# Performance work log

Hardware: AMD Instinct MI355X
Metric: run time of the kernel (lower is better)

The kernel has to match this reference:

```python
import jax, jax.numpy as jnp
import numpy as np

B, T, D = 2, 4096, 1024
H, HD = 16, 64
KV = H * HD  # 1024


def setup_inputs() -> dict:
    key = jax.random.key(0)
    ks = jax.random.split(key, 6)
    sc = lambda k, shape, s: jax.random.normal(k, shape, jnp.float32) * s
    return {
        "x": sc(ks[0], (B, T, D), 1.0),
        "W_in": sc(ks[1], (D, 4 * KV), D ** -0.5),      # in_proj (in, out) layout
        "W_ba": sc(ks[2], (D, 2 * H), D ** -0.5),       # ba_proj
        "conv_w": sc(ks[3], (3 * KV, 1, 4), 0.5),       # depthwise conv, (O, I/groups=1, K)
        "dt_bias": jnp.ones((H,), jnp.float32),
        "A_log": jnp.log(jax.random.uniform(ks[4], (H,), jnp.float32, 1e-3, 16.0)),
        "norm_w": jnp.ones((HD,), jnp.float32),
        "W_o": sc(ks[5], (KV, D), KV ** -0.5),
    }


def _l2norm(t, eps=1e-6):
    return t * jax.lax.rsqrt(jnp.sum(t * t, axis=-1, keepdims=True) + eps)


def reference(x, W_in, W_ba, conv_w, dt_bias, A_log, norm_w, W_o):
    Bb, Tt, _ = x.shape
    qkvz = x @ W_in                                  # [B,T,4*KV]
    q, k, v, z = jnp.split(qkvz, 4, axis=-1)
    b, a = jnp.split(x @ W_ba, 2, axis=-1)           # [B,T,H] each

    # causal depthwise conv (kernel 4, left pad 3) + SiLU on concat(q,k,v)
    qkv = jnp.concatenate([q, k, v], axis=-1).transpose(0, 2, 1)  # [B,3KV,T]
    qkv = jax.lax.conv_general_dilated(
        qkv, conv_w, window_strides=(1,), padding=[(3, 0)],
        feature_group_count=3 * KV, dimension_numbers=("NCH", "OIH", "NCH"))
    qkv = jax.nn.silu(qkv).transpose(0, 2, 1)        # [B,T,3KV]
    q, k, v = jnp.split(qkv, 3, axis=-1)

    rs = lambda t: t.reshape(Bb, Tt, H, HD)
    q, k, v, z = rs(q), rs(k), rs(v), rs(z)

    beta = jax.nn.sigmoid(b)                         # [B,T,H]
    A = jnp.exp(jnp.maximum(A_log, -2.3))            # [H]
    g = -A * jax.nn.softplus(a + dt_bias)            # [B,T,H], log decay <= 0

    # fla use_qk_l2norm_in_kernel=True: l2-normalize q,k; q scaled by d^-0.5
    q = _l2norm(q) * (HD ** -0.5)
    k = _l2norm(k)

    # gated delta rule recurrence over time (state S: [B,H,dk,dv])
    tm = lambda t: jnp.swapaxes(t, 0, 1)             # time-major

    def step(S, inp):
        qt, kt, vt, gt, bt = inp
        S = S * jnp.exp(gt)[..., None, None]
        pred = jnp.einsum("bhk,bhkv->bhv", kt, S)
        S = S + jnp.einsum("bhk,bhv->bhkv", kt, (vt - pred) * bt[..., None])
        o = jnp.einsum("bhk,bhkv->bhv", qt, S)
        return S, o

    S0 = jnp.zeros((Bb, H, HD, HD), jnp.float32)
    _, y = jax.lax.scan(step, S0, (tm(q), tm(k), tm(v), tm(g), tm(beta)))
    y = jnp.swapaxes(y, 0, 1)                        # [B,T,H,HD]

    # RMSNormGated over head_dim, gated by silu(z)
    y = y * jax.lax.rsqrt(jnp.mean(y * y, axis=-1, keepdims=True) + 1e-6)
    y = (norm_w * y) * jax.nn.silu(z)

    return y.reshape(Bb, Tt, KV) @ W_o
```

## Files before the change

kernel.cpp:

```cpp
#include <hip/hip_runtime.h>

typedef unsigned short u16;
typedef unsigned int u32;
typedef __attribute__((ext_vector_type(8))) __bf16 bf16x8;
typedef __attribute__((ext_vector_type(8))) _Float16 f16x8;
typedef __attribute__((ext_vector_type(4))) _Float16 f16x4;
typedef __attribute__((ext_vector_type(4))) float f32x4;

#define DEV __device__ __forceinline__

DEV u16 f2bf(float f) {
  u32 u = __float_as_uint(f);
  u += 0x7FFFu + ((u >> 16) & 1u);
  return (u16)(u >> 16);
}
DEV float bf2f(u16 h) { return __uint_as_float(((u32)h) << 16); }
DEV void splitbf(float f, u16& hi, u16& lo) {
  u16 h = f2bf(f);
  hi = h;
  lo = f2bf(f - bf2f(h));
}
DEV void split4(float4 v, ushort4& hh, ushort4& ll) {
  splitbf(v.x, hh.x, ll.x);
  splitbf(v.y, hh.y, ll.y);
  splitbf(v.z, hh.z, ll.z);
  splitbf(v.w, hh.w, ll.w);
}
DEV int SW(int r, int c) { return r * 64 + ((c) ^ ((r & 7) << 3)); }

DEV int SWG(int r, int c) {
  int db = ((r & 1) << 2) | ((c >> 3) & 3);
  int dbp = db ^ ((r >> 1) & 7);
  return ((r >> 1) << 6) | (dbp << 3) | (c & 7);
}
DEV size_t gidx_swz(size_t row, int col, int rowlen) {
  int rr7 = (int)((row >> 1) & 7);
  int db = (int)(((row & 1) << 2) | ((col >> 3) & 3));
  int dbp = db ^ rr7;
  size_t rowp = (row & ~(size_t)1) | (size_t)(dbp >> 2);
  int colp = (col & ~31) | ((dbp & 3) << 3) | (col & 7);
  return rowp * (size_t)rowlen + colp;
}

#define MFMA16(a,b,c) __builtin_amdgcn_mfma_f32_16x16x32_bf16((a),(b),(c),0,0,0)
#define MFMAH(a,b,c)  __builtin_amdgcn_mfma_f32_16x16x32_f16((a),(b),(c),0,0,0)
#define GLDS16(g,l) __builtin_amdgcn_global_load_lds((__attribute__((address_space(1))) void*)(g), (__attribute__((address_space(3))) void*)(l), 16, 0, 0)

DEV f32x4 mm3(bf16x8 ah, bf16x8 al, bf16x8 bh, bf16x8 bl, f32x4 acc) {
  acc = MFMA16(ah, bl, acc);
  acc = MFMA16(al, bh, acc);
  acc = MFMA16(ah, bh, acc);
  return acc;
}

__global__ __launch_bounds__(256) void k_cast_h(const float* __restrict__ in, _Float16* __restrict__ out, int n) {
  int idx = (blockIdx.x * 256 + threadIdx.x) * 4;
  if (idx + 3 < n) {
    float4 v = *(const float4*)(in + idx);
    f16x4 o = {(_Float16)v.x, (_Float16)v.y, (_Float16)v.z, (_Float16)v.w};
    const size_t row = (size_t)(idx >> 10);
    const int col = idx & 1023;
    *(f16x4*)(out + gidx_swz(row, col, 1024)) = o;
  }
}

__global__ __launch_bounds__(256) void k_transpose_h(const float* __restrict__ in, _Float16* __restrict__ out, int R, int Cc) {
  __shared__ float tile[64][65];
  int c0 = blockIdx.x * 64, r0 = blockIdx.y * 64;
  int lr = threadIdx.x >> 6, lc = threadIdx.x & 63;
#pragma unroll
  for (int i = 0; i < 16; ++i) {
    int r = lr + i * 4;
    tile[r][lc] = in[(size_t)(r0 + r) * Cc + c0 + lc];
  }
  __syncthreads();
#pragma unroll
  for (int i = 0; i < 16; ++i) {
    int oc = lr + i * 4;
    out[gidx_swz((size_t)(c0 + oc), r0 + lc, R)] = (_Float16)tile[lc][oc];
  }
}

__global__ __launch_bounds__(256) void k_transpose(const float* __restrict__ in, u16* __restrict__ out, int R, int Cc) {
  __shared__ float tile[64][65];
  int c0 = blockIdx.x * 64, r0 = blockIdx.y * 64;
  int lr = threadIdx.x >> 6, lc = threadIdx.x & 63;
#pragma unroll
  for (int i = 0; i < 16; ++i) {
    int r = lr + i * 4;
    tile[r][lc] = in[(size_t)(r0 + r) * Cc + c0 + lc];
  }
  __syncthreads();
#pragma unroll
  for (int i = 0; i < 16; ++i) {
    int oc = lr + i * 4;
    out[gidx_swz((size_t)(c0 + oc), r0 + lc, R)] = f2bf(tile[lc][oc]);
  }
}

__global__ __launch_bounds__(512, 2) void k_gemm_h(const _Float16* __restrict__ A, const _Float16* __restrict__ Bt,
                                                   u16* __restrict__ Cq, u16* __restrict__ Cz, int M, int N, int K) {
  __shared__ __align__(16) u16 As[256 * 32];
  __shared__ __align__(16) u16 Bs[256 * 32];
  const int tid = threadIdx.x;
  const int nwg = gridDim.x * gridDim.y;
  int bid = blockIdx.y * gridDim.x + blockIdx.x;
  bid = (bid & 7) * (nwg >> 3) + (bid >> 3);
  const int m0 = (bid / gridDim.x) * 256, n0 = (bid % gridDim.x) * 256;
  const int w = tid >> 6, l = tid & 63;
  const int wr = (w >> 1) * 64, wc = (w & 1) * 128;
  const int lrow = l & 15, lk = (l >> 4) * 8, rbase = (l >> 4) * 4;

  f32x4 acc[4][8];
#pragma unroll
  for (int i = 0; i < 4; ++i)
#pragma unroll
    for (int j = 0; j < 8; ++j) acc[i][j] = {0.f, 0.f, 0.f, 0.f};

  const _Float16* aBase = A + (size_t)m0 * K;
  const _Float16* bBase = Bt + (size_t)n0 * K;
  const int srow0 = tid >> 2, scol0 = (tid & 3) * 8;
  const int srow1 = (tid + 512) >> 2;

  for (int k0 = 0; k0 < K; k0 += 32) {
    __syncthreads();
    GLDS16(aBase + (size_t)srow0 * K + k0 + scol0, &As[tid * 8]);
    GLDS16(aBase + (size_t)srow1 * K + k0 + scol0, &As[4096 + tid * 8]);
    GLDS16(bBase + (size_t)srow0 * K + k0 + scol0, &Bs[tid * 8]);
    GLDS16(bBase + (size_t)srow1 * K + k0 + scol0, &Bs[4096 + tid * 8]);
    __syncthreads();
    f16x8 af[4], bfr[8];
#pragma unroll
    for (int i = 0; i < 4; ++i) af[i] = *(const f16x8*)&As[SWG(wr + i * 16 + lrow, lk)];
#pragma unroll
    for (int j = 0; j < 8; ++j) bfr[j] = *(const f16x8*)&Bs[SWG(wc + j * 16 + lrow, lk)];
#pragma unroll
    for (int i = 0; i < 4; ++i)
#pragma unroll
      for (int j = 0; j < 8; ++j) acc[i][j] = MFMAH(af[i], bfr[j], acc[i][j]);
  }
#pragma unroll
  for (int i = 0; i < 4; ++i)
#pragma unroll
    for (int j = 0; j < 8; ++j)
#pragma unroll
      for (int r = 0; r < 4; ++r) {
        int row = m0 + wr + i * 16 + rbase + r;
        int col = n0 + wc + j * 16 + lrow;
        if (col < 3072) Cq[(size_t)row * 3072 + col] = f2bf(acc[i][j][r]);
        else            Cz[(size_t)row * 1024 + col - 3072] = f2bf(acc[i][j][r]);
      }
}

__global__ __launch_bounds__(256) void k_gemm2(const u16* __restrict__ Ah, const u16* __restrict__ Al,
                                               const u16* __restrict__ Bt, float* __restrict__ Cf,
                                               int M, int N, int K) {
  __shared__ __align__(16) u16 Ash[128 * 32];
  __shared__ __align__(16) u16 Asl[128 * 32];
  __shared__ __align__(16) u16 Bs[128 * 32];
  const int tid = threadIdx.x;
  const int nwg = gridDim.x * gridDim.y;
  int bid = blockIdx.y * gridDim.x + blockIdx.x;
  bid = (bid & 7) * (nwg >> 3) + (bid >> 3);
  const int m0 = (bid / gridDim.x) * 128, n0 = (bid % gridDim.x) * 128;
  const int w = tid >> 6, l = tid & 63;
  const int wr = (w >> 1) * 64, wc = (w & 1) * 64;
  const int lrow = l & 15, lk = (l >> 4) * 8, rbase = (l >> 4) * 4;
  const int srow = tid >> 2, scol = (tid & 3) * 8;

  f32x4 acc[4][4];
#pragma unroll
  for (int i = 0; i < 4; ++i)
#pragma unroll
    for (int j = 0; j < 4; ++j) acc[i][j] = {0.f, 0.f, 0.f, 0.f};

  const u16* ahBase = Ah + (size_t)m0 * K;
  const u16* alBase = Al + (size_t)m0 * K;
  const u16* bBase  = Bt + (size_t)n0 * K;

  for (int k0 = 0; k0 < K; k0 += 32) {
    __syncthreads();
    GLDS16(ahBase + (size_t)srow * K + k0 + scol,        &Ash[tid * 8]);
    GLDS16(ahBase + (size_t)(srow + 64) * K + k0 + scol, &Ash[2048 + tid * 8]);
    GLDS16(alBase + (size_t)srow * K + k0 + scol,        &Asl[tid * 8]);
    GLDS16(alBase + (size_t)(srow + 64) * K + k0 + scol, &Asl[2048 + tid * 8]);
    GLDS16(bBase + (size_t)srow * K + k0 + scol,         &Bs[tid * 8]);
    GLDS16(bBase + (size_t)(srow + 64) * K + k0 + scol,  &Bs[2048 + tid * 8]);
    __syncthreads();
    bf16x8 afh[4], afl[4], bfr[4];
#pragma unroll
    for (int i = 0; i < 4; ++i) afh[i] = *(const bf16x8*)&Ash[SWG(wr + i * 16 + lrow, lk)];
#pragma unroll
    for (int i = 0; i < 4; ++i) afl[i] = *(const bf16x8*)&Asl[SWG(wr + i * 16 + lrow, lk)];
#pragma unroll
    for (int j = 0; j < 4; ++j) bfr[j] = *(const bf16x8*)&Bs[SWG(wc + j * 16 + lrow, lk)];
#pragma unroll
    for (int i = 0; i < 4; ++i)
#pragma unroll
      for (int j = 0; j < 4; ++j) {
        acc[i][j] = MFMA16(afl[i], bfr[j], acc[i][j]);
        acc[i][j] = MFMA16(afh[i], bfr[j], acc[i][j]);
      }
  }
#pragma unroll
  for (int i = 0; i < 4; ++i)
#pragma unroll
    for (int j = 0; j < 4; ++j)
#pragma unroll
      for (int r = 0; r < 4; ++r) {
        int row = m0 + wr + i * 16 + rbase + r;
        int col = n0 + wc + j * 16 + lrow;
        Cf[(size_t)row * N + col] = acc[i][j][r];
      }
}

__global__ __launch_bounds__(256) void k_ba(const float* __restrict__ x, const float* __restrict__ Wba,
                                            const float* __restrict__ dt_bias, const float* __restrict__ A_log,
                                            float* __restrict__ betaO, float* __restrict__ gO) {
  __shared__ float xs[4][1024];
  const int wid = threadIdx.x >> 6, lane = threadIdx.x & 63;
  const int m = blockIdx.x * 4 + wid;
#pragma unroll
  for (int i = 0; i < 16; ++i) xs[wid][lane + 64 * i] = x[(size_t)m * 1024 + lane + 64 * i];
  __syncthreads();
  const int n = lane & 31, half = lane >> 5;
  float acc = 0.f;
  const float* wp = Wba + n;
  const int kk0 = half * 512;
#pragma unroll 8
  for (int kk = kk0; kk < kk0 + 512; ++kk) acc += xs[wid][kk] * wp[kk * 32];
  acc += __shfl_xor(acc, 32);
  if (lane < 32) {
    if (n < 16) {
      betaO[(size_t)m * 16 + n] = 1.f / (1.f + expf(-acc));
    } else {
      int h = n - 16;
      float xx = acc + dt_bias[h];
      float sp = (xx > 20.f) ? xx : log1pf(expf(xx));
      gO[(size_t)m * 16 + h] = -expf(fmaxf(A_log[h], -2.3f)) * sp;
    }
  }
}

__global__ __launch_bounds__(256) void k_conv(const u16* __restrict__ qkv3, const float* __restrict__ convw,
                                              u16* __restrict__ qhG, u16* __restrict__ qlG,
                                              u16* __restrict__ khG, u16* __restrict__ klG,
                                              u16* __restrict__ vhG, u16* __restrict__ vlG) {
  __shared__ float cs[3072];
  __shared__ float innorm[32];
  const int bt = blockIdx.x;
  const int bb = bt >> 12, tt = bt & 4095;
  const int tid = threadIdx.x;
  const size_t rb = (size_t)bb * 4096;
#pragma unroll
  for (int s = 0; s < 3; ++s) {
    const int c4 = tid * 4 + s * 1024;
    float cwa[4][4];
#pragma unroll
    for (int e = 0; e < 4; ++e) {
      float4 t = *(const float4*)&convw[(c4 + e) * 4];
      cwa[e][0] = t.x; cwa[e][1] = t.y; cwa[e][2] = t.z; cwa[e][3] = t.w;
    }
    float acc[4] = {0.f, 0.f, 0.f, 0.f};
#pragma unroll
    for (int j = 0; j < 4; ++j) {
      const int tau = tt - 3 + j;
      if (tau >= 0) {
        ushort4 kv = *(const ushort4*)&qkv3[(rb + tau) * 3072 + c4];
        acc[0] += bf2f(kv.x) * cwa[0][j];
        acc[1] += bf2f(kv.y) * cwa[1][j];
        acc[2] += bf2f(kv.z) * cwa[2][j];
        acc[3] += bf2f(kv.w) * cwa[3][j];
      }
    }
#pragma unroll
    for (int e = 0; e < 4; ++e) cs[c4 + e] = acc[e] / (1.f + expf(-acc[e]));
  }
  __syncthreads();
  {
    const int grp = tid >> 3, off = (tid & 7) * 8;
    const float* p = cs + grp * 64 + off;
    float s = 0.f;
#pragma unroll
    for (int i = 0; i < 8; ++i) s += p[i] * p[i];
    s += __shfl_xor(s, 1); s += __shfl_xor(s, 2); s += __shfl_xor(s, 4);
    if ((tid & 7) == 0) innorm[grp] = rsqrtf(s + 1e-6f);
  }
  __syncthreads();
  const int h = tid >> 4, d4 = (tid & 15) * 4;
  const size_t ob = ((size_t)(bb * 16 + h) * 64 + (tt >> 6)) * 4096 + SW(tt & 63, d4);
  {
    const int ci = h * 64 + d4;
    const float sc = innorm[h] * 0.125f;
    float4 o = {cs[ci] * sc, cs[ci + 1] * sc, cs[ci + 2] * sc, cs[ci + 3] * sc};
    ushort4 hh, ll;
    split4(o, hh, ll);
    *(ushort4*)&qhG[ob] = hh;
    *(ushort4*)&qlG[ob] = ll;
  }
  {
    const int ci = 1024 + h * 64 + d4;
    const float sc = innorm[16 + h];
    float4 o = {cs[ci] * sc, cs[ci + 1] * sc, cs[ci + 2] * sc, cs[ci + 3] * sc};
    ushort4 hh, ll;
    split4(o, hh, ll);
    *(ushort4*)&khG[ob] = hh;
    *(ushort4*)&klG[ob] = ll;
  }
  {
    const int ci = 2048 + h * 64 + d4;
    float4 o = {cs[ci], cs[ci + 1], cs[ci + 2], cs[ci + 3]};
    ushort4 hh, ll;
    split4(o, hh, ll);
    *(ushort4*)&vhG[ob] = hh;
    *(ushort4*)&vlG[ob] = ll;
  }
}

__global__ __launch_bounds__(64) void k_prep(const u16* __restrict__ khG, const u16* __restrict__ klG,
                                             const float* __restrict__ gG, const float* __restrict__ betaG,
                                             float* __restrict__ gcG, u16* __restrict__ Tgh, u16* __restrict__ Tgl) {
  __shared__ __align__(16) char pmem[16384];
  u16* Kbh = (u16*)pmem;
  u16* Kbl = (u16*)(pmem + 8192);
  float* Af = (float*)pmem;
  __shared__ float gcs[64], bs[64];
  const int bhc = blockIdx.x;
  const int c = bhc & 63, h = (bhc >> 6) & 15, bb = bhc >> 10;
  const int lane = threadIdx.x;
  const int t0 = c * 64;
  const size_t rowbase = (size_t)bb * 4096;
  const size_t ktile = (size_t)bhc * 4096;
#pragma unroll
  for (int i = 0; i < 8; ++i) {
    const int idx = lane + 64 * i;
    GLDS16(khG + ktile + idx * 8, &Kbh[idx * 8]);
    GLDS16(klG + ktile + idx * 8, &Kbl[idx * 8]);
  }
  {
    float gv = gG[(rowbase + t0 + lane) * 16 + h];
    float sc = gv;
#pragma unroll
    for (int off = 1; off < 64; off <<= 1) {
      float o = __shfl_up(sc, off);
      if (lane >= off) sc += o;
    }
    gcs[lane] = sc;
    bs[lane] = betaG[(rowbase + t0 + lane) * 16 + h];
    gcG[(size_t)bhc * 64 + lane] = sc;
  }
  __syncthreads();
  const int lrow = lane & 15, lk8 = (lane >> 4) * 8, rbase = (lane >> 4) * 4;
  f32x4 acc[4][4];
#pragma unroll
  for (int i = 0; i < 4; ++i)
#pragma unroll
    for (int j = 0; j < 4; ++j) acc[i][j] = {0.f, 0.f, 0.f, 0.f};
#pragma unroll
  for (int ks = 0; ks < 2; ++ks) {
    bf16x8 afh[4], afl[4], bfh[4], bfl[4];
#pragma unroll
    for (int i = 0; i < 4; ++i) {
      afh[i] = *(const bf16x8*)&Kbh[SW(i * 16 + lrow, ks * 32 + lk8)];
      afl[i] = *(const bf16x8*)&Kbl[SW(i * 16 + lrow, ks * 32 + lk8)];
    }
#pragma unroll
    for (int j = 0; j < 4; ++j) {
      bfh[j] = *(const bf16x8*)&Kbh[SW(j * 16 + lrow, ks * 32 + lk8)];
      bfl[j] = *(const bf16x8*)&Kbl[SW(j * 16 + lrow, ks * 32 + lk8)];
    }
#pragma unroll
    for (int i = 0; i < 4; ++i)
#pragma unroll
      for (int j = 0; j < 4; ++j) acc[i][j] = mm3(afh[i], afl[i], bfh[j], bfl[j], acc[i][j]);
  }
  __syncthreads();
#pragma unroll
  for (int i = 0; i < 4; ++i)
#pragma unroll
    for (int j = 0; j < 4; ++j)
#pragma unroll
      for (int r = 0; r < 4; ++r) {
        int t = i * 16 + rbase + r, s = j * 16 + lrow;
        Af[t * 64 + s] = (s < t) ? bs[t] * expf(gcs[t] - gcs[s]) * acc[i][j][r] : 0.f;
      }
  __syncthreads();
  float x[64];
#pragma unroll
  for (int t = 0; t < 64; ++t) {
    float sum = 0.f;
#pragma unroll
    for (int s4 = 0; s4 + 4 <= t; s4 += 4) {
      float4 a4 = *(const float4*)&Af[t * 64 + s4];
      sum += a4.x * x[s4] + a4.y * x[s4 + 1] + a4.z * x[s4 + 2] + a4.w * x[s4 + 3];
    }
#pragma unroll
    for (int s = (t & ~3); s < t; ++s) sum += Af[t * 64 + s] * x[s];
    x[t] = ((t == lane) ? 1.f : 0.f) - sum;
  }
#pragma unroll
  for (int t = 0; t < 64; ++t) {
    u16 hi, lo;
    splitbf(x[t], hi, lo);
    Tgh[(size_t)bhc * 4096 + SW(t, lane)] = hi;
    Tgl[(size_t)bhc * 4096 + SW(t, lane)] = lo;
  }
}

__global__ __launch_bounds__(256) void k_mn(const u16* __restrict__ khG, const u16* __restrict__ klG,
                                            const u16* __restrict__ vhG, const u16* __restrict__ vlG,
                                            const u16* __restrict__ Tgh, const u16* __restrict__ Tgl,
                                            const float* __restrict__ gcG, const float* __restrict__ betaG,
                                            u16* __restrict__ Mh, u16* __restrict__ Ml,
                                            u16* __restrict__ Nh, u16* __restrict__ Nl) {
  extern __shared__ __align__(16) char smem[];
  u16* base = (u16*)smem;
  u16* Tbh  = base + 0 * 4096;
  u16* Tbl  = base + 1 * 4096;
  u16* X1h  = base + 2 * 4096;
  u16* X1l  = base + 3 * 4096;
  u16* KdTh = base + 4 * 4096;
  u16* KdTl = base + 5 * 4096;
  u16* X2h  = base + 6 * 4096;
  u16* X2l  = base + 7 * 4096;
  float* gcs = (float*)(base + 8 * 4096);
  float* bs  = gcs + 64;

  const int bhc = blockIdx.x;
  const int c = bhc & 63, h = (bhc >> 6) & 15, bb = bhc >> 10;
  const int tid = threadIdx.x, w = tid >> 6, l = tid & 63;
  const int lrow = l & 15, lk8 = (l >> 4) * 8, rbase = (l >> 4) * 4;
  const int t0 = c * 64;
  const size_t rowbase = (size_t)bb * 4096;
  const size_t ktile = (size_t)bhc * 4096;

  if (tid < 64) {
    gcs[tid] = gcG[(size_t)bhc * 64 + tid];
    bs[tid] = betaG[(rowbase + t0 + tid) * 16 + h];
  }
#pragma unroll
  for (int i = 0; i < 2; ++i) {
    const int idx = tid + 256 * i;
    const int off = idx * 8;
    *(float4*)&Tbh[off] = *(const float4*)&Tgh[(size_t)bhc * 4096 + off];
    *(float4*)&Tbl[off] = *(const float4*)&Tgl[(size_t)bhc * 4096 + off];
  }
  __syncthreads();
  const float gc63 = gcs[63];
#pragma unroll
  for (int i = 0; i < 16; ++i) {
    const int flat = tid + 256 * i;
    const int s = flat >> 6, d = flat & 63;
    const int sws = SW(s, d);
    const float kf = bf2f(khG[ktile + sws]) + bf2f(klG[ktile + sws]);
    const float gv = gcs[s], bv = bs[s];
    u16 hh, ll;
    splitbf(bv * expf(gv) * kf, hh, ll);
    X1h[SW(d, s)] = hh; X1l[SW(d, s)] = ll;
    splitbf(expf(gc63 - gv) * kf, hh, ll);
    KdTh[SW(d, s)] = hh; KdTl[SW(d, s)] = ll;
    const float vv = bf2f(vhG[ktile + sws]) + bf2f(vlG[ktile + sws]);
    splitbf(bv * vv, hh, ll);
    X2h[SW(d, s)] = hh; X2l[SW(d, s)] = ll;
  }
  __syncthreads();

  f32x4 aW[4], aU[4];
#pragma unroll
  for (int j = 0; j < 4; ++j) { aW[j] = {0.f,0.f,0.f,0.f}; aU[j] = {0.f,0.f,0.f,0.f}; }
#pragma unroll
  for (int ks = 0; ks < 2; ++ks) {
    const int ao = SW(w * 16 + lrow, ks * 32 + lk8);
    bf16x8 aTh = *(const bf16x8*)&Tbh[ao];
    bf16x8 aTl = *(const bf16x8*)&Tbl[ao];
#pragma unroll
    for (int j = 0; j < 4; ++j) {
      const int bo = SW(j * 16 + lrow, ks * 32 + lk8);
      aW[j] = mm3(aTh, aTl, *(const bf16x8*)&X1h[bo], *(const bf16x8*)&X1l[bo], aW[j]);
      aU[j] = mm3(aTh, aTl, *(const bf16x8*)&X2h[bo], *(const bf16x8*)&X2l[bo], aU[j]);
    }
  }
  __syncthreads();
#pragma unroll
  for (int j = 0; j < 4; ++j)
#pragma unroll
    for (int r = 0; r < 4; ++r) {
      const int t = w * 16 + rbase + r, dcol = j * 16 + lrow;
      u16 hh, ll;
      splitbf(aW[j][r], hh, ll);
      X1h[SW(dcol, t)] = hh; X1l[SW(dcol, t)] = ll;
      splitbf(aU[j][r], hh, ll);
      X2h[SW(dcol, t)] = hh; X2l[SW(dcol, t)] = ll;
    }
  __syncthreads();

  f32x4 aM[4], aN[4];
#pragma unroll
  for (int j = 0; j < 4; ++j) { aM[j] = {0.f,0.f,0.f,0.f}; aN[j] = {0.f,0.f,0.f,0.f}; }
#pragma unroll
  for (int ks = 0; ks < 2; ++ks) {
    const int ao = SW(w * 16 + lrow, ks * 32 + lk8);
    bf16x8 aKh = *(const bf16x8*)&KdTh[ao];
    bf16x8 aKl = *(const bf16x8*)&KdTl[ao];
#pragma unroll
    for (int j = 0; j < 4; ++j) {
      const int bo = SW(j * 16 + lrow, ks * 32 + lk8);
      aM[j] = mm3(aKh, aKl, *(const bf16x8*)&X1h[bo], *(const bf16x8*)&X1l[bo], aM[j]);
      aN[j] = mm3(aKh, aKl, *(const bf16x8*)&X2h[bo], *(const bf16x8*)&X2l[bo], aN[j]);
    }
  }
  __syncthreads();
  const float decC = expf(gc63);
#pragma unroll
  for (int j = 0; j < 4; ++j)
#pragma unroll
    for (int r = 0; r < 4; ++r) {
      const int d = w * 16 + rbase + r, d2 = j * 16 + lrow;
      u16 hh, ll;
      splitbf(((d == d2) ? decC : 0.f) - aM[j][r], hh, ll);
      X1h[SW(d, d2)] = hh; X1l[SW(d, d2)] = ll;
      splitbf(aN[j][r], hh, ll);
      X2h[SW(d, d2)] = hh; X2l[SW(d, d2)] = ll;
    }
  __syncthreads();
#pragma unroll
  for (int i = 0; i < 2; ++i) {
    const int idx = tid + 256 * i;
    const int off = idx * 8;
    *(float4*)&Mh[(size_t)bhc * 4096 + off] = *(const float4*)&X1h[off];
    *(float4*)&Ml[(size_t)bhc * 4096 + off] = *(const float4*)&X1l[off];
    *(float4*)&Nh[(size_t)bhc * 4096 + off] = *(const float4*)&X2h[off];
    *(float4*)&Nl[(size_t)bhc * 4096 + off] = *(const float4*)&X2l[off];
  }
}

__global__ __launch_bounds__(256) void k_seg(const u16* __restrict__ Mh, const u16* __restrict__ Ml,
                                             const u16* __restrict__ Nh, const u16* __restrict__ Nl,
                                             u16* __restrict__ Msegh, u16* __restrict__ Msegl,
                                             u16* __restrict__ Nsegh, u16* __restrict__ Nsegl) {
  extern __shared__ __align__(16) char smem[];
  u16* base = (u16*)smem;
  u16* MaTh = base + 0 * 4096;
  u16* MaTl = base + 1 * 4096;
  u16* NaTh = base + 2 * 4096;
  u16* NaTl = base + 3 * 4096;
  u16* sMh  = base + 4 * 4096;
  u16* sMl  = base + 5 * 4096;
  u16* sNh  = base + 6 * 4096;
  u16* sNl  = base + 7 * 4096;

  const int blk = blockIdx.x;
  const size_t cbase = (size_t)(blk >> 3) * 64 + (blk & 7) * 8;
  const int tid = threadIdx.x, w = tid >> 6, l = tid & 63;
  const int lrow = l & 15, lk8 = (l >> 4) * 8, rbase = (l >> 4) * 4;

#pragma unroll
  for (int i = 0; i < 2; ++i) {
    const int off = (tid + 256 * i) * 8;
    *(float4*)&sMh[off] = *(const float4*)&Mh[cbase * 4096 + off];
    *(float4*)&sMl[off] = *(const float4*)&Ml[cbase * 4096 + off];
    *(float4*)&sNh[off] = *(const float4*)&Nh[cbase * 4096 + off];
    *(float4*)&sNl[off] = *(const float4*)&Nl[cbase * 4096 + off];
  }
  __syncthreads();
#pragma unroll
  for (int i = 0; i < 16; ++i) {
    const int flat = tid + 256 * i;
    const int a = flat >> 6, b = flat & 63;
    MaTh[SW(a, b)] = sMh[SW(b, a)];
    MaTl[SW(a, b)] = sMl[SW(b, a)];
    NaTh[SW(a, b)] = sNh[SW(b, a)];
    NaTl[SW(a, b)] = sNl[SW(b, a)];
  }
  __syncthreads();

  for (int j = 1; j < 8; ++j) {
#pragma unroll
    for (int i = 0; i < 2; ++i) {
      const int off = (tid + 256 * i) * 8;
      *(float4*)&sMh[off] = *(const float4*)&Mh[(cbase + j) * 4096 + off];
      *(float4*)&sMl[off] = *(const float4*)&Ml[(cbase + j) * 4096 + off];
      *(float4*)&sNh[off] = *(const float4*)&Nh[(cbase + j) * 4096 + off];
      *(float4*)&sNl[off] = *(const float4*)&Nl[(cbase + j) * 4096 + off];
    }
    __syncthreads();
    f32x4 aM2[4], aN2[4];
#pragma unroll
    for (int jj = 0; jj < 4; ++jj) { aM2[jj] = {0.f,0.f,0.f,0.f}; aN2[jj] = {0.f,0.f,0.f,0.f}; }
#pragma unroll
    for (int ks = 0; ks < 2; ++ks) {
      const int ao = SW(w * 16 + lrow, ks * 32 + lk8);
      bf16x8 aCh = *(const bf16x8*)&sMh[ao];
      bf16x8 aCl = *(const bf16x8*)&sMl[ao];
#pragma unroll
      for (int jj = 0; jj < 4; ++jj) {
        const int bo = SW(jj * 16 + lrow, ks * 32 + lk8);
        aM2[jj] = mm3(aCh, aCl, *(const bf16x8*)&MaTh[bo], *(const bf16x8*)&MaTl[bo], aM2[jj]);
        aN2[jj] = mm3(aCh, aCl, *(const bf16x8*)&NaTh[bo], *(const bf16x8*)&NaTl[bo], aN2[jj]);
      }
    }
    __syncthreads();
#pragma unroll
    for (int jj = 0; jj < 4; ++jj)
#pragma unroll
      for (int r = 0; r < 4; ++r) {
        const int t = w * 16 + rbase + r, col = jj * 16 + lrow;
        u16 hh, ll;
        splitbf(aM2[jj][r], hh, ll);
        MaTh[SW(col, t)] = hh; MaTl[SW(col, t)] = ll;
        const float nv = aN2[jj][r] + bf2f(sNh[SW(t, col)]) + bf2f(sNl[SW(t, col)]);
        splitbf(nv, hh, ll);
        NaTh[SW(col, t)] = hh; NaTl[SW(col, t)] = ll;
      }
    __syncthreads();
  }
#pragma unroll
  for (int i = 0; i < 16; ++i) {
    const int flat = tid + 256 * i;
    const int t = flat >> 6, s = flat & 63;
    Msegh[(size_t)blk * 4096 + SW(t, s)] = MaTh[SW(s, t)];
    Msegl[(size_t)blk * 4096 + SW(t, s)] = MaTl[SW(s, t)];
    Nsegh[(size_t)blk * 4096 + SW(t, s)] = NaTh[SW(s, t)];
    Nsegl[(size_t)blk * 4096 + SW(t, s)] = NaTl[SW(s, t)];
  }
}

__global__ __launch_bounds__(256) void k_bound(const u16* __restrict__ Msegh, const u16* __restrict__ Msegl,
                                               const u16* __restrict__ Nsegh, const u16* __restrict__ Nsegl,
                                               u16* __restrict__ Ssegh, u16* __restrict__ Ssegl) {
  __shared__ __align__(16) u16 STh[4096], STl[4096];
  __shared__ __align__(16) u16 sMh[4096], sMl[4096], sNh[4096], sNl[4096];
  const int bh = blockIdx.x;
  const int tid = threadIdx.x, w = tid >> 6, l = tid & 63;
  const int lrow = l & 15, lk8 = (l >> 4) * 8, rbase = (l >> 4) * 4;
  for (int i = tid; i < 4096; i += 256) { STh[i] = (u16)0; STl[i] = (u16)0; }
  __syncthreads();
  for (int j = 0; j < 8; ++j) {
    const size_t sb = (size_t)(bh * 8 + j) * 4096;
#pragma unroll
    for (int i = 0; i < 2; ++i) {
      const int off = (tid + 256 * i) * 8;
      *(float4*)&Ssegh[sb + off] = *(const float4*)&STh[off];
      *(float4*)&Ssegl[sb + off] = *(const float4*)&STl[off];
      *(float4*)&sMh[off] = *(const float4*)&Msegh[sb + off];
      *(float4*)&sMl[off] = *(const float4*)&Msegl[sb + off];
      *(float4*)&sNh[off] = *(const float4*)&Nsegh[sb + off];
      *(float4*)&sNl[off] = *(const float4*)&Nsegl[sb + off];
    }
    __syncthreads();
    f32x4 acc[4];
#pragma unroll
    for (int jj = 0; jj < 4; ++jj) acc[jj] = {0.f, 0.f, 0.f, 0.f};
#pragma unroll
    for (int ks = 0; ks < 2; ++ks) {
      const int ao = SW(w * 16 + lrow, ks * 32 + lk8);
      bf16x8 aSh = *(const bf16x8*)&STh[ao];
      bf16x8 aSl = *(const bf16x8*)&STl[ao];
#pragma unroll
      for (int jj = 0; jj < 4; ++jj) {
        const int bo = SW(jj * 16 + lrow, ks * 32 + lk8);
        acc[jj] = mm3(aSh, aSl, *(const bf16x8*)&sMh[bo], *(const bf16x8*)&sMl[bo], acc[jj]);
      }
    }
    __syncthreads();
#pragma unroll
    for (int jj = 0; jj < 4; ++jj)
#pragma unroll
      for (int r = 0; r < 4; ++r) {
        const int v = w * 16 + rbase + r, t = jj * 16 + lrow;
        const float sv = acc[jj][r] + bf2f(sNh[SW(t, v)]) + bf2f(sNl[SW(t, v)]);
        u16 hh, ll;
        splitbf(sv, hh, ll);
        STh[SW(v, t)] = hh; STl[SW(v, t)] = ll;
      }
    __syncthreads();
  }
}

__global__ __launch_bounds__(512, 2) void k_scan2(const u16* __restrict__ qhG, const u16* __restrict__ qlG,
                                               const u16* __restrict__ khG, const u16* __restrict__ klG,
                                               const u16* __restrict__ vhG, const u16* __restrict__ vlG,
                                               const u16* __restrict__ zb,
                                               const u16* __restrict__ Tgh, const u16* __restrict__ Tgl,
                                               const float* __restrict__ gcG,
                                               const float* __restrict__ betaG, const float* __restrict__ norm_w,
                                               const u16* __restrict__ Ssegh, const u16* __restrict__ Ssegl,
                                               u16* __restrict__ Yhi, u16* __restrict__ Ylo) {
  extern __shared__ __align__(16) char smem[];
  u16* base = (u16*)smem;
  u16* Kbh  = base + 0 * 4096;
  u16* Kbl  = base + 1 * 4096;
  u16* Qbh  = base + 2 * 4096;
  u16* Qbl  = base + 3 * 4096;
  u16* Vbh  = base + 4 * 4096;
  u16* Vbl  = base + 5 * 4096;
  u16* Zb   = base + 6 * 4096;
  u16* Tbh  = base + 7 * 4096;
  u16* Tbl  = base + 8 * 4096;
  u16* SbTh = base + 9 * 4096;
  u16* SbTl = base + 10 * 4096;
  u16* Mqh  = base + 11 * 4096;
  u16* Mql  = base + 12 * 4096;
  u16* KdTh = base + 13 * 4096;
  u16* KdTl = base + 14 * 4096;
  u16* RTh  = base + 15 * 4096;
  u16* RTl  = base + 16 * 4096;
  u16* UTh  = base + 17 * 4096;
  u16* UTl  = base + 18 * 4096;
  u16* Ybh  = RTh;
  u16* Ybl  = RTl;
  float* gcs = (float*)(base + 19 * 4096);
  float* bs  = gcs + 64;
  float* nws = gcs + 128;
  float* esF = gcs + 192;
  float* etF = gcs + 256;
  float* ssP = gcs + 320;

  const int blk = blockIdx.x;
  const int bh = blk >> 3, seg = blk & 7;
  const int bb = bh >> 4, h = bh & 15;
  const int tid = threadIdx.x, w = tid >> 6, l = tid & 63;
  const int wrow = w >> 1, jh = w & 1;
  const int lrow = l & 15, lk8 = (l >> 4) * 8, rbase = (l >> 4) * 4;
  const size_t rowbase = (size_t)bb * 4096;
  const size_t bhTile = (size_t)bh * 64;
  const int o8 = tid * 8;
  const int zr = tid >> 3, zc8 = (tid & 7) << 3;

  {
    const int c = seg * 8, t0 = c * 64;
    const size_t gt = (bhTile + c) * 4096;
    GLDS16(qhG + gt + o8, &Qbh[o8]);
    GLDS16(qlG + gt + o8, &Qbl[o8]);
    GLDS16(khG + gt + o8, &Kbh[o8]);
    GLDS16(klG + gt + o8, &Kbl[o8]);
    GLDS16(vhG + gt + o8, &Vbh[o8]);
    GLDS16(vlG + gt + o8, &Vbl[o8]);
    GLDS16(Tgh + (size_t)(bh * 64 + c) * 4096 + o8, &Tbh[o8]);
    GLDS16(Tgl + (size_t)(bh * 64 + c) * 4096 + o8, &Tbl[o8]);
    GLDS16(Ssegh + (size_t)blk * 4096 + o8, &SbTh[o8]);
    GLDS16(Ssegl + (size_t)blk * 4096 + o8, &SbTl[o8]);
    *(float4*)&Zb[SW(zr, zc8)] = *(const float4*)&zb[(rowbase + t0 + zr) * 1024 + h * 64 + zc8];
    if (tid < 64) {
      nws[tid] = norm_w[tid];
      float g0 = gcG[((size_t)bh * 64 + c) * 64 + tid];
      float b0 = betaG[(rowbase + t0 + tid) * 16 + h];
      float g63 = __shfl(g0, 63);
      gcs[tid] = g0; bs[tid] = b0;
      esF[tid] = expf(g63 - g0);
      etF[tid] = expf(g0);
    }
  }
  __syncthreads();

  for (int cc = 0; cc < 8; ++cc) {
    const int c = seg * 8 + cc;
    const int t0 = c * 64;
    const bool pf = (cc < 7);
    const size_t gt1 = (bhTile + c + 1) * 4096;

    float4 pz;
    float pgc = 0.f, pbs = 0.f;
    if (pf) {
      const int t1 = t0 + 64;
      pz = *(const float4*)&zb[(rowbase + t1 + zr) * 1024 + h * 64 + zc8];
      if (tid < 64) {
        pgc = gcG[((size_t)bh * 64 + (c + 1)) * 64 + tid];
        pbs = betaG[(rowbase + t1 + tid) * 16 + h];
      }
    }

#pragma unroll
    for (int i = 0; i < 8; ++i) {
      const int flat = tid * 8 + i;
      const int d = flat >> 6, s = flat & 63;
      const float kv = bf2f(Kbh[SW(s, d)]) + bf2f(Kbl[SW(s, d)]);
      u16 hh, ll;
      splitbf(esF[s] * kv, hh, ll);
      KdTh[SW(d, s)] = hh;
      KdTl[SW(d, s)] = ll;
    }
    f32x4 aqk[2], ap[2], aqs[2];
#pragma unroll
    for (int j = 0; j < 2; ++j) { aqk[j] = {0.f,0.f,0.f,0.f}; ap[j] = {0.f,0.f,0.f,0.f}; aqs[j] = {0.f,0.f,0.f,0.f}; }
#pragma unroll
    for (int ks = 0; ks < 2; ++ks) {
      const int ao = SW(wrow * 16 + lrow, ks * 32 + lk8);
      bf16x8 aKh = *(const bf16x8*)&Kbh[ao];
      bf16x8 aKl = *(const bf16x8*)&Kbl[ao];
      bf16x8 aQh = *(const bf16x8*)&Qbh[ao];
      bf16x8 aQl = *(const bf16x8*)&Qbl[ao];
#pragma unroll
      for (int j = 0; j < 2; ++j) {
        const int jj = jh * 2 + j;
        const int bo = SW(jj * 16 + lrow, ks * 32 + lk8);
        bf16x8 bKh = *(const bf16x8*)&Kbh[bo];
        bf16x8 bKl = *(const bf16x8*)&Kbl[bo];
        bf16x8 bSh = *(const bf16x8*)&SbTh[bo];
        bf16x8 bSl = *(const bf16x8*)&SbTl[bo];
        aqk[j] = mm3(aQh, aQl, bKh, bKl, aqk[j]);
        ap[j]  = mm3(aKh, aKl, bSh, bSl, ap[j]);
        aqs[j] = mm3(aQh, aQl, bSh, bSl, aqs[j]);
      }
    }
#pragma unroll
    for (int j = 0; j < 2; ++j)
#pragma unroll
      for (int r = 0; r < 4; ++r) {
        const int t = wrow * 16 + rbase + r;
        const int s = (jh * 2 + j) * 16 + lrow;
        u16 mh, ml;
        splitbf((s <= t) ? expf(gcs[t] - gcs[s]) * aqk[j][r] : 0.f, mh, ml);
        Mqh[SW(t, s)] = mh;
        Mql[SW(t, s)] = ml;
        const float vv = bf2f(Vbh[SW(t, s)]) + bf2f(Vbl[SW(t, s)]);
        const float rhs = bs[t] * (vv - etF[t] * ap[j][r]);
        u16 rh, rl;
        splitbf(rhs, rh, rl);
        RTh[SW(s, t)] = rh;
        RTl[SW(s, t)] = rl;
      }
    __syncthreads();

    if (pf) {
      GLDS16(qhG + gt1 + o8, &Qbh[o8]);
      GLDS16(qlG + gt1 + o8, &Qbl[o8]);
      GLDS16(khG + gt1 + o8, &Kbh[o8]);
      GLDS16(klG + gt1 + o8, &Kbl[o8]);
      GLDS16(vhG + gt1 + o8, &Vbh[o8]);
      GLDS16(vlG + gt1 + o8, &Vbl[o8]);
    }

    f32x4 au[2];
#pragma unroll
    for (int j = 0; j < 2; ++j) au[j] = {0.f, 0.f, 0.f, 0.f};
#pragma unroll
    for (int ks = 0; ks < 2; ++ks) {
      const int ao = SW(wrow * 16 + lrow, ks * 32 + lk8);
      bf16x8 aTh = *(const bf16x8*)&Tbh[ao];
      bf16x8 aTl = *(const bf16x8*)&Tbl[ao];
#pragma unroll
      for (int j = 0; j < 2; ++j) {
        const int bo = SW((jh * 2 + j) * 16 + lrow, ks * 32 + lk8);
        au[j] = mm3(aTh, aTl, *(const bf16x8*)&RTh[bo], *(const bf16x8*)&RTl[bo], au[j]);
      }
    }
#pragma unroll
    for (int j = 0; j < 2; ++j)
#pragma unroll
      for (int r = 0; r < 4; ++r) {
        u16 uh, ul;
        splitbf(au[j][r], uh, ul);
        const int o = SW((jh * 2 + j) * 16 + lrow, wrow * 16 + rbase + r);
        UTh[o] = uh;
        UTl[o] = ul;
      }
    __syncthreads();

    if (pf) {
      GLDS16(Tgh + (size_t)(bh * 64 + (c + 1)) * 4096 + o8, &Tbh[o8]);
      GLDS16(Tgl + (size_t)(bh * 64 + (c + 1)) * 4096 + o8, &Tbl[o8]);
    }

    f32x4 amu[2], as_[2];
#pragma unroll
    for (int j = 0; j < 2; ++j) { amu[j] = {0.f,0.f,0.f,0.f}; as_[j] = {0.f,0.f,0.f,0.f}; }
#pragma unroll
    for (int ks = 0; ks < 2; ++ks) {
      const int ao = SW(wrow * 16 + lrow, ks * 32 + lk8);
      bf16x8 aMh = *(const bf16x8*)&Mqh[ao];
      bf16x8 aMl = *(const bf16x8*)&Mql[ao];
      bf16x8 aKdh = *(const bf16x8*)&KdTh[ao];
      bf16x8 aKdl = *(const bf16x8*)&KdTl[ao];
#pragma unroll
      for (int j = 0; j < 2; ++j) {
        const int bo = SW((jh * 2 + j) * 16 + lrow, ks * 32 + lk8);
        bf16x8 bUh = *(const bf16x8*)&UTh[bo];
        bf16x8 bUl = *(const bf16x8*)&UTl[bo];
        amu[j] = mm3(aMh, aMl, bUh, bUl, amu[j]);
        as_[j] = mm3(aKdh, aKdl, bUh, bUl, as_[j]);
      }
    }
    float yv_[4][2];
#pragma unroll
    for (int r = 0; r < 4; ++r) {
      const int t = wrow * 16 + rbase + r;
      const float gt = etF[t];
      float ss = 0.f;
#pragma unroll
      for (int j = 0; j < 2; ++j) {
        yv_[r][j] = gt * aqs[j][r] + amu[j][r];
        ss += yv_[r][j] * yv_[r][j];
      }
      ss += __shfl_xor(ss, 1); ss += __shfl_xor(ss, 2); ss += __shfl_xor(ss, 4); ss += __shfl_xor(ss, 8);
      if (lrow == 0) ssP[jh * 64 + t] = ss;
    }
    __syncthreads();
#pragma unroll
    for (int r = 0; r < 4; ++r) {
      const int t = wrow * 16 + rbase + r;
      const float rstd = rsqrtf((ssP[t] + ssP[64 + t]) * (1.f / 64.f) + 1e-6f);
#pragma unroll
      for (int j = 0; j < 2; ++j) {
        const int col = (jh * 2 + j) * 16 + lrow;
        const float zz = bf2f(Zb[SW(t, col)]);
        const float yv = yv_[r][j] * rstd * nws[col] * (zz / (1.f + expf(-zz)));
        u16 yh, yl;
        splitbf(yv, yh, yl);
        Ybh[SW(t, col)] = yh;
        Ybl[SW(t, col)] = yl;
      }
    }
    {
      const float decC = etF[63];
#pragma unroll
      for (int j = 0; j < 2; ++j)
#pragma unroll
        for (int r = 0; r < 4; ++r) {
          const int d = wrow * 16 + rbase + r, col = (jh * 2 + j) * 16 + lrow;
          const int o = SW(col, d);
          const float s0 = bf2f(SbTh[o]) + bf2f(SbTl[o]);
          const float sv = decC * s0 + as_[j][r];
          u16 sh, sl;
          splitbf(sv, sh, sl);
          SbTh[o] = sh;
          SbTl[o] = sl;
        }
    }
    __syncthreads();

    {
      const size_t gsw = gidx_swz(rowbase + t0 + zr, h * 64 + zc8, 1024);
      *(float4*)&Yhi[gsw] = *(const float4*)&Ybh[SW(zr, zc8)];
      *(float4*)&Ylo[gsw] = *(const float4*)&Ybl[SW(zr, zc8)];
    }
    if (pf) {
      *(float4*)&Zb[SW(zr, zc8)] = pz;
      if (tid < 64) {
        float g63 = __shfl(pgc, 63);
        gcs[tid] = pgc; bs[tid] = pbs;
        esF[tid] = expf(g63 - pgc);
        etF[tid] = expf(pgc);
      }
    }
    __syncthreads();
  }
}

extern "C" void kernel_launch(void* const* d_in, const int* in_sizes, int n_in,
                              void* d_out, int out_size, void* d_ws, size_t ws_size,
                              hipStream_t stream) {
  (void)in_sizes; (void)n_in; (void)out_size; (void)ws_size;
  const float* x       = (const float*)d_in[0];
  const float* W_in    = (const float*)d_in[1];
  const float* W_ba    = (const float*)d_in[2];
  const float* conv_w  = (const float*)d_in[3];
  const float* dt_bias = (const float*)d_in[4];
  const float* A_log   = (const float*)d_in[5];
  const float* norm_w  = (const float*)d_in[6];
  const float* W_o     = (const float*)d_in[7];
  float* out = (float*)d_out;
  char* ws = (char*)d_ws;
  const size_t MB = 1048576;

  _Float16* xh = (_Float16*)(ws + 0);
  u16* MhB   = (u16*)(ws + 0);
  u16* YhiB  = (u16*)(ws + 0);
  u16* MlB   = (u16*)(ws + 16 * MB);
  u16* YloB  = (u16*)(ws + 16 * MB);
  _Float16* WinT = (_Float16*)(ws + 32 * MB);
  float* gB  = (float*)(ws + 32 * MB);
  float* bB  = (float*)(ws + 32 * MB + 524288);
  float* gcB = (float*)(ws + 33 * MB);
  u16* Ssegh = (u16*)(ws + 34 * MB);
  u16* Ssegl = (u16*)(ws + 36 * MB);
  u16* Msegh = (u16*)(ws + 38 * MB);
  u16* Msegl = (u16*)(ws + 40 * MB);
  u16* Nsegh = (u16*)(ws + 42 * MB);
  u16* Nsegl = (u16*)(ws + 44 * MB);
  u16* WoT   = (u16*)(ws + 48 * MB);
  u16* qkv3  = (u16*)(ws + 50 * MB);
  u16* NhB   = (u16*)(ws + 50 * MB);
  u16* NlB   = (u16*)(ws + 66 * MB);
  u16* zbB   = (u16*)(ws + 98 * MB);
  u16* qhG   = (u16*)(ws + 114 * MB);
  u16* qlG   = (u16*)(ws + 130 * MB);
  u16* khG   = (u16*)(ws + 146 * MB);
  u16* klG   = (u16*)(ws + 162 * MB);
  u16* vhG   = (u16*)(ws + 178 * MB);
  u16* vlG   = (u16*)(ws + 194 * MB);
  u16* TghB  = (u16*)(ws + 210 * MB);
  u16* TglB  = (u16*)(ws + 226 * MB);

  const int SCAN_LDS = 19 * 8192 + 448 * 4;
  const int MN_LDS   = 8 * 8192 + 512;
  const int SEG_LDS  = 8 * 8192;

  k_cast_h<<<8192, 256, 0, stream>>>(x, xh, 8388608);
  k_transpose_h<<<dim3(64, 16), 256, 0, stream>>>(W_in, WinT, 1024, 4096);
  k_transpose<<<dim3(16, 16), 256, 0, stream>>>(W_o, WoT, 1024, 1024);
  k_gemm_h<<<dim3(16, 32), 512, 0, stream>>>(xh, WinT, qkv3, zbB, 8192, 4096, 1024);
  k_ba<<<2048, 256, 0, stream>>>(x, W_ba, dt_bias, A_log, bB, gB);
  k_conv<<<8192, 256, 0, stream>>>(qkv3, conv_w, qhG, qlG, khG, klG, vhG, vlG);
  k_prep<<<2048, 64, 0, stream>>>(khG, klG, gB, bB, gcB, TghB, TglB);
  hipFuncSetAttribute((const void*)k_mn, hipFuncAttributeMaxDynamicSharedMemorySize, MN_LDS);
  k_mn<<<2048, 256, MN_LDS, stream>>>(khG, klG, vhG, vlG, TghB, TglB, gcB, bB, MhB, MlB, NhB, NlB);
  hipFuncSetAttribute((const void*)k_seg, hipFuncAttributeMaxDynamicSharedMemorySize, SEG_LDS);
  k_seg<<<256, 256, SEG_LDS, stream>>>(MhB, MlB, NhB, NlB, Msegh, Msegl, Nsegh, Nsegl);
  k_bound<<<32, 256, 0, stream>>>(Msegh, Msegl, Nsegh, Nsegl, Ssegh, Ssegl);
  hipFuncSetAttribute((const void*)k_scan2, hipFuncAttributeMaxDynamicSharedMemorySize, SCAN_LDS);
  k_scan2<<<256, 512, SCAN_LDS, stream>>>(qhG, qlG, khG, klG, vhG, vlG, zbB, TghB, TglB, gcB, bB, norm_w,
                                          Ssegh, Ssegl, YhiB, YloB);
  k_gemm2<<<dim3(8, 64), 256, 0, stream>>>(YhiB, YloB, WoT, out, 8192, 1024, 1024);
}
```

Measured before the change: 530.9 us.

## Double-buffer LDS tiles in both GEMM kernels to overlap loads with MFMA

```diff
diff --git a/kernel.cpp b/kernel.cpp
--- a/kernel.cpp
+++ b/kernel.cpp
@@ -100,8 +100,8 @@
 
 __global__ __launch_bounds__(512, 2) void k_gemm_h(const _Float16* __restrict__ A, const _Float16* __restrict__ Bt,
                                                    u16* __restrict__ Cq, u16* __restrict__ Cz, int M, int N, int K) {
-  __shared__ __align__(16) u16 As[256 * 32];
-  __shared__ __align__(16) u16 Bs[256 * 32];
+  __shared__ __align__(16) u16 As[2][256 * 32];
+  __shared__ __align__(16) u16 Bs[2][256 * 32];
   const int tid = threadIdx.x;
   const int nwg = gridDim.x * gridDim.y;
   int bid = blockIdx.y * gridDim.x + blockIdx.x;
@@ -122,22 +122,29 @@
   const int srow0 = tid >> 2, scol0 = (tid & 3) * 8;
   const int srow1 = (tid + 512) >> 2;
 
+  auto STAGE = [&](int buf, int k0) {
+    GLDS16(aBase + (size_t)srow0 * K + k0 + scol0, &As[buf][tid * 8]);
+    GLDS16(aBase + (size_t)srow1 * K + k0 + scol0, &As[buf][4096 + tid * 8]);
+    GLDS16(bBase + (size_t)srow0 * K + k0 + scol0, &Bs[buf][tid * 8]);
+    GLDS16(bBase + (size_t)srow1 * K + k0 + scol0, &Bs[buf][4096 + tid * 8]);
+  };
+
+  STAGE(0, 0);
+  __syncthreads();
+  int cur = 0;
   for (int k0 = 0; k0 < K; k0 += 32) {
-    __syncthreads();
-    GLDS16(aBase + (size_t)srow0 * K + k0 + scol0, &As[tid * 8]);
-    GLDS16(aBase + (size_t)srow1 * K + k0 + scol0, &As[4096 + tid * 8]);
-    GLDS16(bBase + (size_t)srow0 * K + k0 + scol0, &Bs[tid * 8]);
-    GLDS16(bBase + (size_t)srow1 * K + k0 + scol0, &Bs[4096 + tid * 8]);
-    __syncthreads();
+    if (k0 + 32 < K) STAGE(cur ^ 1, k0 + 32);
     f16x8 af[4], bfr[8];
 #pragma unroll
-    for (int i = 0; i < 4; ++i) af[i] = *(const f16x8*)&As[SWG(wr + i * 16 + lrow, lk)];
-#pragma unroll
-    for (int j = 0; j < 8; ++j) bfr[j] = *(const f16x8*)&Bs[SWG(wc + j * 16 + lrow, lk)];
+    for (int i = 0; i < 4; ++i) af[i] = *(const f16x8*)&As[cur][SWG(wr + i * 16 + lrow, lk)];
+#pragma unroll
+    for (int j = 0; j < 8; ++j) bfr[j] = *(const f16x8*)&Bs[cur][SWG(wc + j * 16 + lrow, lk)];
 #pragma unroll
     for (int i = 0; i < 4; ++i)
 #pragma unroll
       for (int j = 0; j < 8; ++j) acc[i][j] = MFMAH(af[i], bfr[j], acc[i][j]);
+    __syncthreads();
+    cur ^= 1;
   }
 #pragma unroll
   for (int i = 0; i < 4; ++i)
@@ -152,12 +159,12 @@
       }
 }
 
-__global__ __launch_bounds__(256) void k_gemm2(const u16* __restrict__ Ah, const u16* __restrict__ Al,
+__global__ __launch_bounds__(256, 2) void k_gemm2(const u16* __restrict__ Ah, const u16* __restrict__ Al,
                                                const u16* __restrict__ Bt, float* __restrict__ Cf,
                                                int M, int N, int K) {
-  __shared__ __align__(16) u16 Ash[128 * 32];
-  __shared__ __align__(16) u16 Asl[128 * 32];
-  __shared__ __align__(16) u16 Bs[128 * 32];
+  __shared__ __align__(16) u16 Ash[2][128 * 32];
+  __shared__ __align__(16) u16 Asl[2][128 * 32];
+  __shared__ __align__(16) u16 Bs[2][128 * 32];
   const int tid = threadIdx.x;
   const int nwg = gridDim.x * gridDim.y;
   int bid = blockIdx.y * gridDim.x + blockIdx.x;
@@ -178,22 +185,27 @@
   const u16* alBase = Al + (size_t)m0 * K;
   const u16* bBase  = Bt + (size_t)n0 * K;
 
+  auto STAGE = [&](int buf, int k0) {
+    GLDS16(ahBase + (size_t)srow * K + k0 + scol,        &Ash[buf][tid * 8]);
+    GLDS16(ahBase + (size_t)(srow + 64) * K + k0 + scol, &Ash[buf][2048 + tid * 8]);
+    GLDS16(alBase + (size_t)srow * K + k0 + scol,        &Asl[buf][tid * 8]);
+    GLDS16(alBase + (size_t)(srow + 64) * K + k0 + scol, &Asl[buf][2048 + tid * 8]);
+    GLDS16(bBase + (size_t)srow * K + k0 + scol,         &Bs[buf][tid * 8]);
+    GLDS16(bBase + (size_t)(srow + 64) * K + k0 + scol,  &Bs[buf][2048 + tid * 8]);
+  };
+
+  STAGE(0, 0);
+  __syncthreads();
+  int cur = 0;
   for (int k0 = 0; k0 < K; k0 += 32) {
-    __syncthreads();
-    GLDS16(ahBase + (size_t)srow * K + k0 + scol,        &Ash[tid * 8]);
-    GLDS16(ahBase + (size_t)(srow + 64) * K + k0 + scol, &Ash[2048 + tid * 8]);
-    GLDS16(alBase + (size_t)srow * K + k0 + scol,        &Asl[tid * 8]);
-    GLDS16(alBase + (size_t)(srow + 64) * K + k0 + scol, &Asl[2048 + tid * 8]);
-    GLDS16(bBase + (size_t)srow * K + k0 + scol,         &Bs[tid * 8]);
-    GLDS16(bBase + (size_t)(srow + 64) * K + k0 + scol,  &Bs[2048 + tid * 8]);
-    __syncthreads();
+    if (k0 + 32 < K) STAGE(cur ^ 1, k0 + 32);
     bf16x8 afh[4], afl[4], bfr[4];
 #pragma unroll
-    for (int i = 0; i < 4; ++i) afh[i] = *(const bf16x8*)&Ash[SWG(wr + i * 16 + lrow, lk)];
-#pragma unroll
-    for (int i = 0; i < 4; ++i) afl[i] = *(const bf16x8*)&Asl[SWG(wr + i * 16 + lrow, lk)];
-#pragma unroll
-    for (int j = 0; j < 4; ++j) bfr[j] = *(const bf16x8*)&Bs[SWG(wc + j * 16 + lrow, lk)];
+    for (int i = 0; i < 4; ++i) afh[i] = *(const bf16x8*)&Ash[cur][SWG(wr + i * 16 + lrow, lk)];
+#pragma unroll
+    for (int i = 0; i < 4; ++i) afl[i] = *(const bf16x8*)&Asl[cur][SWG(wr + i * 16 + lrow, lk)];
+#pragma unroll
+    for (int j = 0; j < 4; ++j) bfr[j] = *(const bf16x8*)&Bs[cur][SWG(wc + j * 16 + lrow, lk)];
 #pragma unroll
     for (int i = 0; i < 4; ++i)
 #pragma unroll
@@ -201,6 +213,8 @@
         acc[i][j] = MFMA16(afl[i], bfr[j], acc[i][j]);
         acc[i][j] = MFMA16(afh[i], bfr[j], acc[i][j]);
       }
+    __syncthreads();
+    cur ^= 1;
   }
 #pragma unroll
   for (int i = 0; i < 4; ++i)
```

After: 512.9 us (median of 2 runs). 3.4% less time.
